# Performance work log

Hardware: AMD Instinct MI355X
Metric: run time of the kernel (lower is better)

The kernel has to match this reference:

```python
import jax, jax.numpy as jnp
import numpy as np

N_NODES = 100000
N_EDGES = 3200000
HID = 32
HEADS = 2
EDGE_IN = 4
NEG_SLOPE = 0.2  # PyG GATConv default


def gat_conv(x, src, dst, W, att_src, att_dst, bias, heads, out_ch, concat):
    """PyG-style GATConv with self-loops already included in (src, dst).
    x: [N, in], W: [in, heads*out_ch], att_*: [heads, out_ch], bias: [heads*out_ch] or [out_ch]."""
    N = x.shape[0]
    h = (x @ W).reshape(N, heads, out_ch)                      # [N,H,C]
    a_src = jnp.einsum('nhc,hc->nh', h, att_src)               # [N,H]
    a_dst = jnp.einsum('nhc,hc->nh', h, att_dst)
    e = a_src[src] + a_dst[dst]                                # [E,H]
    e = jnp.where(e > 0, e, NEG_SLOPE * e)                     # leaky_relu
    # segment softmax over incoming edges of each dst node
    m = jax.ops.segment_max(e, dst, num_segments=N)            # [N,H]
    ex = jnp.exp(e - m[dst])
    s = jax.ops.segment_sum(ex, dst, num_segments=N)
    alpha = ex / (s[dst] + 1e-16)                              # [E,H]
    msg = h[src] * alpha[:, :, None]                           # [E,H,C]
    out = jax.ops.segment_sum(msg, dst, num_segments=N)        # [N,H,C]
    out = out.reshape(N, heads * out_ch) if concat else out.mean(axis=1)
    return out + bias


def setup_inputs() -> dict:
    key = jax.random.key(0)
    ks = jax.random.split(key, 16)
    x = jax.random.normal(ks[0], (N_NODES, 1), dtype=jnp.float32)
    edge_index = jax.random.randint(ks[1], (2, N_EDGES), 0, N_NODES, dtype=jnp.int32)
    edge_attr = jax.random.uniform(ks[2], (N_EDGES, EDGE_IN), dtype=jnp.float32)
    g = lambda k, shape, fan: (jax.random.normal(k, shape, dtype=jnp.float32) / np.sqrt(fan)).astype(jnp.float32)
    params = {
        'W1': g(ks[3], (1, HEADS * HID), 1),
        'att_src1': g(ks[4], (HEADS, HID), HID),
        'att_dst1': g(ks[5], (HEADS, HID), HID),
        'b1': jnp.zeros((HEADS * HID,), jnp.float32),
        'W2': g(ks[6], (HEADS * HID, HID), HEADS * HID),
        'att_src2': g(ks[7], (1, HID), HID),
        'att_dst2': g(ks[8], (1, HID), HID),
        'b2': jnp.zeros((HID,), jnp.float32),
        'Wm1': g(ks[9], (2 * HID + EDGE_IN, 32), 2 * HID + EDGE_IN),
        'bm1': jnp.zeros((32,), jnp.float32),
        'Wm2': g(ks[10], (32, 16), 32),
        'bm2': jnp.zeros((16,), jnp.float32),
        'Wm3': g(ks[11], (16, 1), 16),
        'bm3': jnp.zeros((1,), jnp.float32),
    }
    return {'x': x, 'edge_index': edge_index, 'edge_attr': edge_attr, **params}


def reference(x, edge_index, edge_attr, W1, att_src1, att_dst1, b1, W2, att_src2, att_dst2, b2,
              Wm1, bm1, Wm2, bm2, Wm3, bm3):
    N = x.shape[0]
    # PyG GATConv adds self-loops by default
    loop = jnp.arange(N, dtype=edge_index.dtype)
    src = jnp.concatenate([edge_index[0], loop])
    dst = jnp.concatenate([edge_index[1], loop])
    out = gat_conv(x, src, dst, W1, att_src1, att_dst1, b1, HEADS, HID, concat=True)
    out = jax.nn.relu(out)
    node_embs = gat_conv(out, src, dst, W2, att_src2, att_dst2, b2, 1, HID, concat=False)  # [N,HID]
    # edge scorer on ORIGINAL edges (no self-loops)
    e_src, e_dst = edge_index[0], edge_index[1]
    feat = jnp.concatenate([node_embs[e_src], node_embs[e_dst], edge_attr], axis=1)  # [E, 2*HID+4]
    h = jax.nn.relu(feat @ Wm1 + bm1)   # dropout is identity in eval mode
    h = jax.nn.relu(h @ Wm2 + bm2)
    scores = jax.nn.sigmoid(h @ Wm3 + bm3)
    return scores.squeeze(-1)
```

## Files before the change

kernel.cpp:

```cpp
#include <hip/hip_runtime.h>
#include <math.h>

#define NN 100000
#define NE 3200000
#define NEG 0.2f
#define NBKT 391
#define TILE_E 8192
#define BCAP 12288
#define K6_BLOCKS 3125

typedef __attribute__((ext_vector_type(8))) short bf16x8;
typedef __attribute__((ext_vector_type(4))) float f32x4;

__device__ __forceinline__ float leaky(float v) { return v > 0.f ? v : NEG * v; }

__device__ __forceinline__ unsigned int f2bf(float f) {
    unsigned int u = __float_as_uint(f);
    return (u + 0x7fffu + ((u >> 16) & 1u)) >> 16;
}
__device__ __forceinline__ float bf2f(unsigned short h) {
    return __uint_as_float(((unsigned int)h) << 16);
}

__global__ void __launch_bounds__(256) kA1_part(const int* __restrict__ ei,
                                                int* __restrict__ bktcnt,
                                                int* __restrict__ ebuf) {
    __shared__ int cnt[NBKT];
    __shared__ int eofs[NBKT];
    __shared__ int cur[NBKT];
    __shared__ int lcur[NBKT];
    __shared__ int sh[512];
    __shared__ int lstage[TILE_E];
    __shared__ unsigned short lbkt[TILE_E];
    int t = threadIdx.x;
    for (int i = t; i < NBKT; i += 256) cnt[i] = 0;
    __syncthreads();
    int base = blockIdx.x * TILE_E;
    int m = min(TILE_E, NE - base);
    int tq = m >> 10;
    const int4* d4 = (const int4*)(ei + NE + base);
    const int4* s4 = (const int4*)(ei + base);
    int4 dd[8];
#pragma unroll
    for (int q = 0; q < 8; ++q) {
        if (q < tq) {
            int4 v = d4[q * 256 + t];
            dd[q] = v;
            atomicAdd(&cnt[v.x >> 8], 1);
            atomicAdd(&cnt[v.y >> 8], 1);
            atomicAdd(&cnt[v.z >> 8], 1);
            atomicAdd(&cnt[v.w >> 8], 1);
        }
    }
    __syncthreads();
    sh[t] = (t < NBKT) ? cnt[t] : 0;
    sh[t + 256] = (t + 256 < NBKT) ? cnt[t + 256] : 0;
    __syncthreads();
    for (int o = 1; o < 512; o <<= 1) {
        int a0 = (t >= o) ? sh[t - o] : 0;
        int a1 = ((t + 256) >= o) ? sh[t + 256 - o] : 0;
        __syncthreads();
        sh[t] += a0;
        sh[t + 256] += a1;
        __syncthreads();
    }
    for (int i = t; i < NBKT; i += 256) {
        int c = cnt[i];
        int e = sh[i] - c;
        eofs[i] = e;
        lcur[i] = e;
        cur[i] = c ? atomicAdd(&bktcnt[i], c) : 0;
    }
    __syncthreads();
#pragma unroll
    for (int q = 0; q < 8; ++q) {
        if (q < tq) {
            int4 sv = s4[q * 256 + t];
            int4 dv = dd[q];
            int b, p;
            b = dv.x >> 8; p = atomicAdd(&lcur[b], 1);
            lstage[p] = (sv.x << 8) | (dv.x & 255); lbkt[p] = (unsigned short)b;
            b = dv.y >> 8; p = atomicAdd(&lcur[b], 1);
            lstage[p] = (sv.y << 8) | (dv.y & 255); lbkt[p] = (unsigned short)b;
            b = dv.z >> 8; p = atomicAdd(&lcur[b], 1);
            lstage[p] = (sv.z << 8) | (dv.z & 255); lbkt[p] = (unsigned short)b;
            b = dv.w >> 8; p = atomicAdd(&lcur[b], 1);
            lstage[p] = (sv.w << 8) | (dv.w & 255); lbkt[p] = (unsigned short)b;
        }
    }
    __syncthreads();
    for (int i = t; i < m; i += 256) {
        int b = lbkt[i];
        int p = cur[b] + (i - eofs[b]);
        if (p < BCAP) ebuf[b * BCAP + p] = lstage[i];
    }
}

__global__ void __launch_bounds__(512) kscan(const int* __restrict__ bktcnt,
                                             int* __restrict__ bktoff,
                                             int* __restrict__ rowst,
                                             const float* __restrict__ W1,
                                             const float* __restrict__ as1,
                                             const float* __restrict__ ad1,
                                             float* __restrict__ c4) {
    int t = threadIdx.x;
    if (t < 2) {
        float cs = 0.f, cd = 0.f;
        for (int c = 0; c < 32; ++c) {
            float w = W1[t * 32 + c];
            cs += w * as1[t * 32 + c];
            cd += w * ad1[t * 32 + c];
        }
        c4[t] = cs;
        c4[2 + t] = cd;
    }
    __shared__ int sh[512];
    int v = (t < NBKT) ? min(bktcnt[t], BCAP) : 0;
    sh[t] = v;
    __syncthreads();
    for (int o = 1; o < 512; o <<= 1) {
        int add = (t >= o) ? sh[t - o] : 0;
        __syncthreads();
        sh[t] += add;
        __syncthreads();
    }
    if (t < NBKT) bktoff[t] = sh[t] - v;
    if (t == 511) {
        bktoff[NBKT] = sh[511];
        rowst[NN] = sh[511];
    }
}

__global__ void __launch_bounds__(256) kB_sort(const int* __restrict__ bktcnt,
                                               const int* __restrict__ bktoff,
                                               const int* __restrict__ ebuf,
                                               int* __restrict__ rowst,
                                               int* __restrict__ srcidx) {
    __shared__ int cnt[256];
    __shared__ int tmp[256];
    __shared__ int lstage[BCAP];
    int b = blockIdx.x, t = threadIdx.x;
    int n = min(bktcnt[b], BCAP);
    int obase = bktoff[b];
    const int* ib = ebuf + b * BCAP;
    const int4* ib4 = (const int4*)ib;
    int nq = n >> 2;
    cnt[t] = 0;
    __syncthreads();
    for (int i = t; i < nq; i += 256) {
        int4 v = ib4[i];
        atomicAdd(&cnt[v.x & 255], 1);
        atomicAdd(&cnt[v.y & 255], 1);
        atomicAdd(&cnt[v.z & 255], 1);
        atomicAdd(&cnt[v.w & 255], 1);
    }
    for (int i = (nq << 2) + t; i < n; i += 256)
        atomicAdd(&cnt[ib[i] & 255], 1);
    __syncthreads();
    int v = cnt[t];
    tmp[t] = v;
    __syncthreads();
    for (int o = 1; o < 256; o <<= 1) {
        int add = (t >= o) ? tmp[t - o] : 0;
        __syncthreads();
        tmp[t] += add;
        __syncthreads();
    }
    int excl = tmp[t] - v;
    int node = (b << 8) + t;
    if (node < NN) rowst[node] = obase + excl;
    cnt[t] = excl;
    __syncthreads();
    for (int i = t; i < nq; i += 256) {
        int4 e4 = ib4[i];
        int p;
        p = atomicAdd(&cnt[e4.x & 255], 1); lstage[p] = e4.x >> 8;
        p = atomicAdd(&cnt[e4.y & 255], 1); lstage[p] = e4.y >> 8;
        p = atomicAdd(&cnt[e4.z & 255], 1); lstage[p] = e4.z >> 8;
        p = atomicAdd(&cnt[e4.w & 255], 1); lstage[p] = e4.w >> 8;
    }
    for (int i = (nq << 2) + t; i < n; i += 256) {
        int e = ib[i];
        int p = atomicAdd(&cnt[e & 255], 1);
        lstage[p] = e >> 8;
    }
    __syncthreads();
    for (int i = t; i < n; i += 256)
        srcidx[obase + i] = lstage[i];
}

__global__ void __launch_bounds__(256) k_agg1(const int* __restrict__ rowstart,
                                              const int* __restrict__ srcidx,
                                              const float* __restrict__ x,
                                              const float* __restrict__ c4,
                                              float2* __restrict__ r2) {
    int gtid = blockIdx.x * blockDim.x + threadIdx.x;
    int n = gtid >> 4;
    int lane = gtid & 15;
    if (n >= NN) return;
    float c0 = c4[0], c1 = c4[1], c2 = c4[2], c3 = c4[3];
    float xd = x[n];
    float xdc2 = xd * c2, xdc3 = xd * c3;
    float s0 = 0.f, s1 = 0.f, t0 = 0.f, t1 = 0.f;
    int rs = rowstart[n], re = rowstart[n + 1];
    for (int i = rs + lane; i < re; i += 16) {
        float xs = x[__builtin_nontemporal_load(srcidx + i)];
        float ex0 = __expf(leaky(xs * c0 + xdc2));
        float ex1 = __expf(leaky(xs * c1 + xdc3));
        s0 += ex0;
        s1 += ex1;
        t0 += ex0 * xs;
        t1 += ex1 * xs;
    }
#pragma unroll
    for (int m = 8; m >= 1; m >>= 1) {
        s0 += __shfl_xor(s0, m, 16);
        s1 += __shfl_xor(s1, m, 16);
        t0 += __shfl_xor(t0, m, 16);
        t1 += __shfl_xor(t1, m, 16);
    }
    if (lane == 0) {
        float ex0 = __expf(leaky(xd * (c0 + c2)));
        float ex1 = __expf(leaky(xd * (c1 + c3)));
        s0 += ex0;
        s1 += ex1;
        t0 += ex0 * xd;
        t1 += ex1 * xd;
        r2[n] = make_float2(t0 / (s0 + 1e-16f), t1 / (s1 + 1e-16f));
    }
}

__global__ void __launch_bounds__(256) k3_node(const float2* __restrict__ r2,
                                               const float* __restrict__ W1,
                                               const float* __restrict__ b1,
                                               const float* __restrict__ W2,
                                               const float* __restrict__ as2,
                                               const float* __restrict__ ad2,
                                               unsigned int* __restrict__ h8,
                                               float2* __restrict__ a2) {
    int n = blockIdx.x * blockDim.x + threadIdx.x;
    if (n >= NN) return;
    float2 r = r2[n];
    float h2[32];
#pragma unroll
    for (int c = 0; c < 32; ++c) h2[c] = 0.f;
    for (int j = 0; j < 64; ++j) {
        float o = W1[j] * (j < 32 ? r.x : r.y) + b1[j];
        o = fmaxf(o, 0.f);
#pragma unroll
        for (int c = 0; c < 32; ++c) h2[c] += o * W2[j * 32 + c];
    }
    float asum = 0.f, adsum = 0.f;
#pragma unroll
    for (int c = 0; c < 32; ++c) {
        asum += h2[c] * as2[c];
        adsum += h2[c] * ad2[c];
    }
    a2[n] = make_float2(asum, adsum);
    unsigned int w[8];
#pragma unroll
    for (int q = 0; q < 8; ++q) {
        int v = __builtin_amdgcn_cvt_pk_fp8_f32(h2[q * 4 + 0], h2[q * 4 + 1], 0, false);
        v = __builtin_amdgcn_cvt_pk_fp8_f32(h2[q * 4 + 2], h2[q * 4 + 3], v, true);
        w[q] = (unsigned int)v;
    }
    uint4* hg = (uint4*)(h8 + (size_t)n * 8);
    hg[0] = make_uint4(w[0], w[1], w[2], w[3]);
    hg[1] = make_uint4(w[4], w[5], w[6], w[7]);
}

__global__ void __launch_bounds__(256) k_agg2(const int* __restrict__ rowstart,
                                              const int* __restrict__ srcidx,
                                              const unsigned char* __restrict__ h8,
                                              const float2* __restrict__ a2,
                                              const float* __restrict__ b2,
                                              unsigned short* __restrict__ embq) {
    __shared__ int loff[256];
    __shared__ float lex[256];
    int tid = threadIdx.x;
    int gtid = blockIdx.x * 256 + tid;
    int n = gtid >> 5;
    int c = gtid & 31;
    if (n >= NN) return;
    int wbase = tid & ~31;
    float2 an = a2[n];
    float adn = an.y;
    float exn = __expf(leaky(an.x + adn));
    float u = exn * __builtin_amdgcn_cvt_f32_fp8(h8[((unsigned)n << 5) + c], 0);
    float lsum = 0.f;
    int rs = rowstart[n], re = rowstart[n + 1];
    for (int base = rs; base < re; base += 32) {
        int cnt = re - base;
        int off = 0;
        float exj = 0.f;
        if (c < cnt) {
            int sjv = __builtin_nontemporal_load(srcidx + base + c);
            off = sjv << 5;
            float2 asrc = a2[sjv];
            exj = __expf(leaky(asrc.x + adn));
            lsum += exj;
        }
        loff[tid] = off;
        asm volatile("s_waitcnt lgkmcnt(0)" ::: "memory");
        int4 ov[8];
#pragma unroll
        for (int q = 0; q < 8; ++q) ov[q] = ((const int4*)(loff + wbase))[q];
        unsigned int hb[32];
#pragma unroll
        for (int q = 0; q < 8; ++q) {
            hb[4 * q + 0] = h8[ov[q].x + c];
            hb[4 * q + 1] = h8[ov[q].y + c];
            hb[4 * q + 2] = h8[ov[q].z + c];
            hb[4 * q + 3] = h8[ov[q].w + c];
        }
        lex[tid] = exj;
        asm volatile("s_waitcnt lgkmcnt(0)" ::: "memory");
#pragma unroll
        for (int q = 0; q < 8; ++q) {
            float4 ev = ((const float4*)(lex + wbase))[q];
            u += ev.x * __builtin_amdgcn_cvt_f32_fp8(hb[4 * q + 0], 0);
            u += ev.y * __builtin_amdgcn_cvt_f32_fp8(hb[4 * q + 1], 0);
            u += ev.z * __builtin_amdgcn_cvt_f32_fp8(hb[4 * q + 2], 0);
            u += ev.w * __builtin_amdgcn_cvt_f32_fp8(hb[4 * q + 3], 0);
        }
    }
#pragma unroll
    for (int m = 16; m >= 1; m >>= 1) lsum += __shfl_xor(lsum, m, 32);
    float ssum = lsum + exn;
    embq[((unsigned)n << 5) + c] = (unsigned short)f2bf(u / (ssum + 1e-16f) + b2[c]);
}

__global__ void __launch_bounds__(256) k6_mfma(const int* __restrict__ ei,
                                               const float* __restrict__ ea,
                                               const unsigned short* __restrict__ embq,
                                               const float* __restrict__ Wm1,
                                               const float* __restrict__ bm1,
                                               const float* __restrict__ Wm2,
                                               const float* __restrict__ bm2,
                                               const float* __restrict__ Wm3,
                                               const float* __restrict__ bm3,
                                               float* __restrict__ out) {
    __shared__ unsigned short ldsq[4][4 * 640];
    int tid = threadIdx.x;
    int wave = tid >> 6, lane = tid & 63;
    int m = lane & 15, quad = lane >> 4;
    unsigned short* wl = ldsq[wave];
    float* wz = (float*)wl;

    bf16x8 B1[3][2];
#pragma unroll
    for (int c = 0; c < 3; ++c) {
#pragma unroll
        for (int t = 0; t < 2; ++t) {
            bf16x8 v;
#pragma unroll
            for (int j = 0; j < 8; ++j) {
                int kk = c * 32 + quad * 8 + j;
                float w = (kk < 68) ? Wm1[kk * 32 + 2 * m + t] : 0.f;
                v[j] = (short)f2bf(w);
            }
            B1[c][t] = v;
        }
    }
    bf16x8 B2;
#pragma unroll
    for (int j = 0; j < 8; ++j)
        B2[j] = (short)f2bf(Wm2[(quad * 8 + j) * 16 + m]);
    float bl = bm1[2 * m], bh = bm1[2 * m + 1];
    float b2v = bm2[m], w3v = Wm3[m], b3 = bm3[0];

    int gw = blockIdx.x * 4 + wave;

    int s2[2][4], d2[2][4];
    f32x4 ev2[2][4];
    bf16x8 A0[2][4], A1[2][4];

    auto LOADIDX = [&](int b, int ii) {
#pragma unroll
        for (int u = 0; u < 4; ++u) {
            int e = (gw * 16 + ii * 4) * 16 + u * 16 + m;
            s2[b][u] = __builtin_nontemporal_load(ei + e);
            d2[b][u] = __builtin_nontemporal_load(ei + NE + e);
            if (quad == 0)
                ev2[b][u] = __builtin_nontemporal_load((const f32x4*)ea + e);
        }
    };
    auto GATHER = [&](int b) {
#pragma unroll
        for (int u = 0; u < 4; ++u) {
            A0[b][u] = *(const bf16x8*)(embq + (((unsigned)s2[b][u] << 5) + quad * 8));
            A1[b][u] = *(const bf16x8*)(embq + (((unsigned)d2[b][u] << 5) + quad * 8));
        }
    };

    LOADIDX(0, 0);
    GATHER(0);
    LOADIDX(1, 1);

#pragma unroll
    for (int ii = 0; ii < 4; ++ii) {
        const int b = ii & 1;
        int eb0 = (gw * 16 + ii * 4) * 16;
#pragma unroll
        for (int u = 0; u < 4; ++u) {
            bf16x8 z = {0, 0, 0, 0, 0, 0, 0, 0};
            if (quad == 0) {
                f32x4 av = ev2[b][u];
                z[0] = (short)f2bf(av[0]);
                z[1] = (short)f2bf(av[1]);
                z[2] = (short)f2bf(av[2]);
                z[3] = (short)f2bf(av[3]);
            }
            f32x4 accL = {bl, bl, bl, bl};
            f32x4 accH = {bh, bh, bh, bh};
            accL = __builtin_amdgcn_mfma_f32_16x16x32_bf16(A0[b][u], B1[0][0], accL, 0, 0, 0);
            accH = __builtin_amdgcn_mfma_f32_16x16x32_bf16(A0[b][u], B1[0][1], accH, 0, 0, 0);
            accL = __builtin_amdgcn_mfma_f32_16x16x32_bf16(A1[b][u], B1[1][0], accL, 0, 0, 0);
            accH = __builtin_amdgcn_mfma_f32_16x16x32_bf16(A1[b][u], B1[1][1], accH, 0, 0, 0);
            accL = __builtin_amdgcn_mfma_f32_16x16x32_bf16(z, B1[2][0], accL, 0, 0, 0);
            accH = __builtin_amdgcn_mfma_f32_16x16x32_bf16(z, B1[2][1], accH, 0, 0, 0);
#pragma unroll
            for (int r = 0; r < 4; ++r) {
                int row = quad * 4 + r;
                unsigned int uL = __float_as_uint(fmaxf(accL[r], 0.f)) + 0x8000u;
                unsigned int uH = __float_as_uint(fmaxf(accH[r], 0.f)) + 0x8000u;
                unsigned int packed = __builtin_amdgcn_perm(uH, uL, 0x07060302);
                *(unsigned int*)(wl + u * 640 + row * 40 + 2 * m) = packed;
            }
        }
        if (ii < 3) GATHER(b ^ 1);
        if (ii < 2) LOADIDX(b, ii + 2);
        asm volatile("s_waitcnt lgkmcnt(0)" ::: "memory");
#pragma unroll
        for (int u = 0; u < 4; ++u) {
            bf16x8 aq = *(const bf16x8*)(wl + u * 640 + m * 40 + quad * 8);
            f32x4 accO = {b2v, b2v, b2v, b2v};
            accO = __builtin_amdgcn_mfma_f32_16x16x32_bf16(aq, B2, accO, 0, 0, 0);
#pragma unroll
            for (int r = 0; r < 4; ++r) {
                int edge = u * 16 + quad * 4 + r;
                wz[edge * 20 + m] = fmaxf(accO[r], 0.f) * w3v;
            }
        }
        asm volatile("s_waitcnt lgkmcnt(0)" ::: "memory");
        {
            f32x4 p0 = *(const f32x4*)(wz + lane * 20 + 0);
            f32x4 p1 = *(const f32x4*)(wz + lane * 20 + 4);
            f32x4 p2 = *(const f32x4*)(wz + lane * 20 + 8);
            f32x4 p3 = *(const f32x4*)(wz + lane * 20 + 12);
            float sum = ((p0[0] + p0[1]) + (p0[2] + p0[3])) +
                        ((p1[0] + p1[1]) + (p1[2] + p1[3])) +
                        ((p2[0] + p2[1]) + (p2[2] + p2[3])) +
                        ((p3[0] + p3[1]) + (p3[2] + p3[3]));
            float sc = 1.f / (1.f + __expf(-(sum + b3)));
            __builtin_nontemporal_store(sc, out + eb0 + lane);
        }
        asm volatile("" ::: "memory");
    }
}

extern "C" void kernel_launch(void* const* d_in, const int* in_sizes, int n_in,
                              void* d_out, int out_size, void* d_ws, size_t ws_size,
                              hipStream_t stream) {
    const float* x   = (const float*)d_in[0];
    const int* ei    = (const int*)d_in[1];
    const float* ea  = (const float*)d_in[2];
    const float* W1  = (const float*)d_in[3];
    const float* as1 = (const float*)d_in[4];
    const float* ad1 = (const float*)d_in[5];
    const float* b1  = (const float*)d_in[6];
    const float* W2  = (const float*)d_in[7];
    const float* as2 = (const float*)d_in[8];
    const float* ad2 = (const float*)d_in[9];
    const float* b2  = (const float*)d_in[10];
    const float* Wm1 = (const float*)d_in[11];
    const float* bm1 = (const float*)d_in[12];
    const float* Wm2 = (const float*)d_in[13];
    const float* bm2 = (const float*)d_in[14];
    const float* Wm3 = (const float*)d_in[15];
    const float* bm3 = (const float*)d_in[16];
    float* out = (float*)d_out;

    char* ws = (char*)d_ws;
    float* c4      = (float*)(ws + 0);
    int*   bktcnt  = (int*)  (ws + 256);
    int*   bktoff  = (int*)  (ws + 2048);
    int*   rowst   = (int*)  (ws + 5632);
    float* r2      = (float*)(ws + 405760);
    float* a2      = (float*)(ws + 1205760);
    int*   ebufP   = (int*)  (ws + 2005760);
    int*   srcidx  = (int*)  (ws + 21224192);
    unsigned char* h8    = (unsigned char*)ebufP;
    unsigned short* embq = (unsigned short*)(ws + 34024192);

    const int NB = (NN + 255) / 256;
    const int TB = (NE + TILE_E - 1) / TILE_E;

    hipMemsetAsync(bktcnt, 0, NBKT * sizeof(int), stream);
    hipLaunchKernelGGL(kA1_part, dim3(TB), dim3(256), 0, stream, ei, bktcnt, ebufP);
    hipLaunchKernelGGL(kscan, dim3(1), dim3(512), 0, stream, bktcnt, bktoff, rowst,
                       W1, as1, ad1, c4);
    hipLaunchKernelGGL(kB_sort, dim3(NBKT), dim3(256), 0, stream, bktcnt, bktoff, ebufP,
                       rowst, srcidx);
    hipLaunchKernelGGL(k_agg1, dim3((NN * 16 + 255) / 256), dim3(256), 0, stream,
                       rowst, srcidx, x, c4, (float2*)r2);
    hipLaunchKernelGGL(k3_node, dim3(NB), dim3(256), 0, stream, (float2*)r2, W1, b1, W2,
                       as2, ad2, (unsigned int*)h8, (float2*)a2);
    hipLaunchKernelGGL(k_agg2, dim3((NN * 32 + 255) / 256), dim3(256), 0, stream,
                       rowst, srcidx, h8, (float2*)a2, b2, embq);
    hipLaunchKernelGGL(k6_mfma, dim3(K6_BLOCKS), dim3(256), 0, stream, ei, ea, embq,
                       Wm1, bm1, Wm2, bm2, Wm3, bm3, out);
}
```

Baseline: 333.7 us.

## Quantize node embeddings to int8 and use i8 MFMA in edge scorer

Adds a global abs-max reduction in k_agg2 and a new k_quant kernel that converts the bf16 node embeddings to per-tensor int8. The edge MLP's first layer then gathers 32-byte int8 rows instead of 64-byte bf16 rows and runs i32 int8 MFMAs with per-column weight scales, dequantizing into the bf16 edge-attribute accumulator. This halves gather traffic in the dominant edge kernel, at the cost of an extra kernel launch, an atomic reduction, and reduced numerical precision.

```diff
diff --git a/kernel.cpp b/kernel.cpp
--- a/kernel.cpp
+++ b/kernel.cpp
@@ -11,6 +11,7 @@
 
 typedef __attribute__((ext_vector_type(8))) short bf16x8;
 typedef __attribute__((ext_vector_type(4))) float f32x4;
+typedef __attribute__((ext_vector_type(4))) int i32x4;
 
 __device__ __forceinline__ float leaky(float v) { return v > 0.f ? v : NEG * v; }
 
@@ -274,7 +275,8 @@
                                               const unsigned char* __restrict__ h8,
                                               const float2* __restrict__ a2,
                                               const float* __restrict__ b2,
-                                              unsigned short* __restrict__ embq) {
+                                              unsigned short* __restrict__ embq,
+                                              float* __restrict__ gmaxp) {
     __shared__ int loff[256];
     __shared__ float lex[256];
     int tid = threadIdx.x;
@@ -327,12 +329,50 @@
 #pragma unroll
     for (int m = 16; m >= 1; m >>= 1) lsum += __shfl_xor(lsum, m, 32);
     float ssum = lsum + exn;
-    embq[((unsigned)n << 5) + c] = (unsigned short)f2bf(u / (ssum + 1e-16f) + b2[c]);
+    float av = u / (ssum + 1e-16f) + b2[c];
+    embq[((unsigned)n << 5) + c] = (unsigned short)f2bf(av);
+    float am = fabsf(av);
+#pragma unroll
+    for (int mm = 32; mm >= 1; mm >>= 1) am = fmaxf(am, __shfl_xor(am, mm));
+    if ((tid & 63) == 0) atomicMax((int*)gmaxp, __float_as_int(am));
+}
+
+__global__ void __launch_bounds__(256) k_quant(const unsigned short* __restrict__ embq,
+                                               const float* __restrict__ gmaxp,
+                                               unsigned char* __restrict__ embq8) {
+    int n = blockIdx.x * 256 + threadIdx.x;
+    if (n >= NN) return;
+    float s = 127.f / fmaxf(*gmaxp, 1e-20f);
+    const uint4* src = (const uint4*)(embq + ((size_t)n << 5));
+    uint4 rr[2] = {src[0], src[1]};
+    uint4 r2v = src[2], r3v = src[3];
+    unsigned int w[8];
+    auto q2 = [&](unsigned int uu) -> unsigned int {
+        float a = bf2f((unsigned short)(uu & 0xffff));
+        float b = bf2f((unsigned short)(uu >> 16));
+        int qa = (int)rintf(a * s);
+        int qb = (int)rintf(b * s);
+        qa = max(-127, min(127, qa));
+        qb = max(-127, min(127, qb));
+        return ((unsigned)qa & 255u) | (((unsigned)qb & 255u) << 8);
+    };
+    w[0] = q2(rr[0].x) | (q2(rr[0].y) << 16);
+    w[1] = q2(rr[0].z) | (q2(rr[0].w) << 16);
+    w[2] = q2(rr[1].x) | (q2(rr[1].y) << 16);
+    w[3] = q2(rr[1].z) | (q2(rr[1].w) << 16);
+    w[4] = q2(r2v.x) | (q2(r2v.y) << 16);
+    w[5] = q2(r2v.z) | (q2(r2v.w) << 16);
+    w[6] = q2(r3v.x) | (q2(r3v.y) << 16);
+    w[7] = q2(r3v.z) | (q2(r3v.w) << 16);
+    uint4* dst = (uint4*)(embq8 + ((size_t)n << 5));
+    dst[0] = make_uint4(w[0], w[1], w[2], w[3]);
+    dst[1] = make_uint4(w[4], w[5], w[6], w[7]);
 }
 
 __global__ void __launch_bounds__(256) k6_mfma(const int* __restrict__ ei,
                                                const float* __restrict__ ea,
-                                               const unsigned short* __restrict__ embq,
+                                               const unsigned char* __restrict__ embq8,
+                                               const float* __restrict__ gmaxp,
                                                const float* __restrict__ Wm1,
                                                const float* __restrict__ bm1,
                                                const float* __restrict__ Wm2,
@@ -347,19 +387,60 @@
     unsigned short* wl = ldsq[wave];
     float* wz = (float*)wl;
 
-    bf16x8 B1[3][2];
-#pragma unroll
-    for (int c = 0; c < 3; ++c) {
+    const float sE = (*gmaxp) * (1.f / 127.f);
+
+    bf16x8 B1ea[2];
+#pragma unroll
+    for (int t = 0; t < 2; ++t) {
+        bf16x8 v;
+#pragma unroll
+        for (int j = 0; j < 8; ++j) {
+            int kk = 64 + quad * 8 + j;
+            float w = (kk < 68) ? Wm1[kk * 32 + 2 * m + t] : 0.f;
+            v[j] = (short)f2bf(w);
+        }
+        B1ea[t] = v;
+    }
+    float wv[2][2][8];
+    float cmax0 = 0.f, cmax1 = 0.f;
+#pragma unroll
+    for (int c = 0; c < 2; ++c) {
 #pragma unroll
         for (int t = 0; t < 2; ++t) {
-            bf16x8 v;
 #pragma unroll
             for (int j = 0; j < 8; ++j) {
-                int kk = c * 32 + quad * 8 + j;
-                float w = (kk < 68) ? Wm1[kk * 32 + 2 * m + t] : 0.f;
-                v[j] = (short)f2bf(w);
+                float w = Wm1[(c * 32 + quad * 8 + j) * 32 + 2 * m + t];
+                wv[c][t][j] = w;
+                if (t == 0) cmax0 = fmaxf(cmax0, fabsf(w));
+                else        cmax1 = fmaxf(cmax1, fabsf(w));
             }
-            B1[c][t] = v;
+        }
+    }
+    cmax0 = fmaxf(cmax0, __shfl_xor(cmax0, 16));
+    cmax0 = fmaxf(cmax0, __shfl_xor(cmax0, 32));
+    cmax1 = fmaxf(cmax1, __shfl_xor(cmax1, 16));
+    cmax1 = fmaxf(cmax1, __shfl_xor(cmax1, 32));
+    long W8[2][2];
+    float invS[2];
+    {
+        float s0 = 127.f / fmaxf(cmax0, 1e-20f);
+        float s1 = 127.f / fmaxf(cmax1, 1e-20f);
+        invS[0] = cmax0 * (1.f / 127.f) * sE;
+        invS[1] = cmax1 * (1.f / 127.f) * sE;
+#pragma unroll
+        for (int c = 0; c < 2; ++c) {
+#pragma unroll
+            for (int t = 0; t < 2; ++t) {
+                float sc = t ? s1 : s0;
+                unsigned int lo = 0, hi = 0;
+#pragma unroll
+                for (int j = 0; j < 4; ++j)
+                    lo |= ((unsigned)((int)rintf(wv[c][t][j] * sc) & 255)) << (8 * j);
+#pragma unroll
+                for (int j = 4; j < 8; ++j)
+                    hi |= ((unsigned)((int)rintf(wv[c][t][j] * sc) & 255)) << (8 * (j - 4));
+                W8[c][t] = (long)(((unsigned long long)hi << 32) | lo);
+            }
         }
     }
     bf16x8 B2;
@@ -373,7 +454,7 @@
 
     int s2[2][4], d2[2][4];
     f32x4 ev2[2][4];
-    bf16x8 A0[2][4], A1[2][4];
+    long A0l[2][4], A1l[2][4];
 
     auto LOADIDX = [&](int b, int ii) {
 #pragma unroll
@@ -388,8 +469,8 @@
     auto GATHER = [&](int b) {
 #pragma unroll
         for (int u = 0; u < 4; ++u) {
-            A0[b][u] = *(const bf16x8*)(embq + (((unsigned)s2[b][u] << 5) + quad * 8));
-            A1[b][u] = *(const bf16x8*)(embq + (((unsigned)d2[b][u] << 5) + quad * 8));
+            A0l[b][u] = *(const long*)(embq8 + (((unsigned)s2[b][u]) * 32u) + quad * 8);
+            A1l[b][u] = *(const long*)(embq8 + (((unsigned)d2[b][u]) * 32u) + quad * 8);
         }
     };
 
@@ -411,19 +492,23 @@
                 z[2] = (short)f2bf(av[2]);
                 z[3] = (short)f2bf(av[3]);
             }
+            i32x4 aIL = {0, 0, 0, 0};
+            i32x4 aIH = {0, 0, 0, 0};
+            aIL = __builtin_amdgcn_mfma_i32_16x16x32_i8(A0l[b][u], W8[0][0], aIL, 0, 0, 0);
+            aIL = __builtin_amdgcn_mfma_i32_16x16x32_i8(A1l[b][u], W8[1][0], aIL, 0, 0, 0);
+            aIH = __builtin_amdgcn_mfma_i32_16x16x32_i8(A0l[b][u], W8[0][1], aIH, 0, 0, 0);
+            aIH = __builtin_amdgcn_mfma_i32_16x16x32_i8(A1l[b][u], W8[1][1], aIH, 0, 0, 0);
             f32x4 accL = {bl, bl, bl, bl};
             f32x4 accH = {bh, bh, bh, bh};
-            accL = __builtin_amdgcn_mfma_f32_16x16x32_bf16(A0[b][u], B1[0][0], accL, 0, 0, 0);
-            accH = __builtin_amdgcn_mfma_f32_16x16x32_bf16(A0[b][u], B1[0][1], accH, 0, 0, 0);
-            accL = __builtin_amdgcn_mfma_f32_16x16x32_bf16(A1[b][u], B1[1][0], accL, 0, 0, 0);
-            accH = __builtin_amdgcn_mfma_f32_16x16x32_bf16(A1[b][u], B1[1][1], accH, 0, 0, 0);
-            accL = __builtin_amdgcn_mfma_f32_16x16x32_bf16(z, B1[2][0], accL, 0, 0, 0);
-            accH = __builtin_amdgcn_mfma_f32_16x16x32_bf16(z, B1[2][1], accH, 0, 0, 0);
+            accL = __builtin_amdgcn_mfma_f32_16x16x32_bf16(z, B1ea[0], accL, 0, 0, 0);
+            accH = __builtin_amdgcn_mfma_f32_16x16x32_bf16(z, B1ea[1], accH, 0, 0, 0);
 #pragma unroll
             for (int r = 0; r < 4; ++r) {
                 int row = quad * 4 + r;
-                unsigned int uL = __float_as_uint(fmaxf(accL[r], 0.f)) + 0x8000u;
-                unsigned int uH = __float_as_uint(fmaxf(accH[r], 0.f)) + 0x8000u;
+                float hL = accL[r] + (float)aIL[r] * invS[0];
+                float hH = accH[r] + (float)aIH[r] * invS[1];
+                unsigned int uL = __float_as_uint(fmaxf(hL, 0.f)) + 0x8000u;
+                unsigned int uH = __float_as_uint(fmaxf(hH, 0.f)) + 0x8000u;
                 unsigned int packed = __builtin_amdgcn_perm(uH, uL, 0x07060302);
                 *(unsigned int*)(wl + u * 640 + row * 40 + 2 * m) = packed;
             }
@@ -483,6 +568,7 @@
 
     char* ws = (char*)d_ws;
     float* c4      = (float*)(ws + 0);
+    float* gmax    = (float*)(ws + 128);
     int*   bktcnt  = (int*)  (ws + 256);
     int*   bktoff  = (int*)  (ws + 2048);
     int*   rowst   = (int*)  (ws + 5632);
@@ -491,12 +577,14 @@
     int*   ebufP   = (int*)  (ws + 2005760);
     int*   srcidx  = (int*)  (ws + 21224192);
     unsigned char* h8    = (unsigned char*)ebufP;
+    unsigned char* embq8 = (unsigned char*)(ws + 2005760 + 3200000);
     unsigned short* embq = (unsigned short*)(ws + 34024192);
 
     const int NB = (NN + 255) / 256;
     const int TB = (NE + TILE_E - 1) / TILE_E;
 
     hipMemsetAsync(bktcnt, 0, NBKT * sizeof(int), stream);
+    hipMemsetAsync(gmax, 0, sizeof(float), stream);
     hipLaunchKernelGGL(kA1_part, dim3(TB), dim3(256), 0, stream, ei, bktcnt, ebufP);
     hipLaunchKernelGGL(kscan, dim3(1), dim3(512), 0, stream, bktcnt, bktoff, rowst,
                        W1, as1, ad1, c4);
@@ -507,7 +595,8 @@
     hipLaunchKernelGGL(k3_node, dim3(NB), dim3(256), 0, stream, (float2*)r2, W1, b1, W2,
                        as2, ad2, (unsigned int*)h8, (float2*)a2);
     hipLaunchKernelGGL(k_agg2, dim3((NN * 32 + 255) / 256), dim3(256), 0, stream,
-                       rowst, srcidx, h8, (float2*)a2, b2, embq);
-    hipLaunchKernelGGL(k6_mfma, dim3(K6_BLOCKS), dim3(256), 0, stream, ei, ea, embq,
-                       Wm1, bm1, Wm2, bm2, Wm3, bm3, out);
-}
+                       rowst, srcidx, h8, (float2*)a2, b2, embq, gmax);
+    hipLaunchKernelGGL(k_quant, dim3(NB), dim3(256), 0, stream, embq, gmax, embq8);
+    hipLaunchKernelGGL(k6_mfma, dim3(K6_BLOCKS), dim3(256), 0, stream, ei, ea, embq8,
+                       gmax, Wm1, bm1, Wm2, bm2, Wm3, bm3, out);
+}
```

After: 864.8 us. 2.59x slower.
